# Kernel optimization log

Hardware: AMD Instinct MI355X
Metric: run time of the kernel (lower is better)

## Reference

```python
import jax, jax.numpy as jnp
import numpy as np

B, F, S, H = 8, 512, 8192, 8
D = F // H
GROUPS = F // 16  # GroupNorm group_cnt = channels // 16
EPS = 1e-8


def group_norm(x, gamma, beta):
    # x: [B, C, S]; normalize per (group-channels, spatial) like torch GroupNorm
    b, c, s = x.shape
    xg = x.reshape(b, GROUPS, c // GROUPS, s)
    mu = xg.mean(axis=(2, 3), keepdims=True)
    var = xg.var(axis=(2, 3), keepdims=True)
    xn = ((xg - mu) * jax.lax.rsqrt(var + EPS)).reshape(b, c, s)
    return xn * gamma[None, :, None] + beta[None, :, None]


def setup_inputs() -> dict:
    key = jax.random.key(0)
    ks = jax.random.split(key, 5)
    return {
        "hidden_states": jax.random.normal(ks[0], (B, F, S), jnp.float32),
        "qkv_w": jax.random.normal(ks[1], (3, H, D, F), jnp.float32) * 0.02,
        "qkv_b": jnp.zeros((3, 1, 1, H, D), jnp.float32),
        "out_proj": jax.random.normal(ks[2], (F, F), jnp.float32) * 0.02,
        "gn1_gamma": jnp.ones((F,), jnp.float32),
        "gn1_beta": jnp.zeros((F,), jnp.float32),
        "gn2_gamma": jnp.ones((F,), jnp.float32),
        "gn2_beta": jnp.zeros((F,), jnp.float32),
        # torch init is zeros; use small random so the gated branch is exercised
        "gate_g": jax.random.normal(ks[3], (F, 1), jnp.float32) * 0.1,
    }


def reference(hidden_states, qkv_w, qkv_b, out_proj,
              gn1_gamma, gn1_beta, gn2_gamma, gn2_beta, gate_g):
    x = group_norm(hidden_states, gn1_gamma, gn1_beta)
    # [3, B, S, H, D]
    qkv = jnp.einsum('bfl,ihdf->iblhd', x, qkv_w) + qkv_b
    q = jax.nn.elu(qkv[0]) + 1.0
    k = jax.nn.elu(qkv[1]) + 1.0
    v = qkv[2]
    # global non-causal linear attention: KV = sum_l k_l v_l^T  -> [B,H,D,D]
    kv = jnp.einsum('blhf,blhF->bhFf', k, v)
    k_sum = jnp.sum(k, axis=1, keepdims=True)               # [B,1,H,D]
    z = jnp.sum(q * k_sum, axis=-1, keepdims=True)          # [B,S,H,1]
    qz = q / z
    out = jnp.einsum('blhf,bhFf->blhF', qz, kv)             # [B,S,H,D]
    out = out.reshape(out.shape[0], out.shape[1], -1)       # [B,S,F]
    y = jnp.einsum('blf,Ff->bFl', out, out_proj)            # [B,F,S]
    y = group_norm(y, gn2_gamma, gn2_beta)
    # rezero-style gate: residual + per-channel gate * branch
    return hidden_states + gate_g[None] * y
```

## Files before the change

### kernel.cpp

```cpp
#include <hip/hip_runtime.h>
#include <hip/hip_bf16.h>

#define BB 8
#define FF 512
#define SS 8192
#define HH 8
#define DD 64
#define N1 1536

typedef __hip_bfloat16 bf16;
typedef __attribute__((ext_vector_type(8))) short bf16x8;
typedef __attribute__((ext_vector_type(4))) float f32x4;

__device__ __forceinline__ float us2f(unsigned short u) {
    union { unsigned int i; float f; } x; x.i = ((unsigned int)u) << 16; return x.f;
}
__device__ __forceinline__ unsigned short f2b(float f) {
    unsigned int u = __builtin_bit_cast(unsigned int, f);
    return (unsigned short)((u + 0x7FFFu + ((u >> 16) & 1u)) >> 16);
}
__device__ __forceinline__ void gll16(const void* g, void* l) {
    __builtin_amdgcn_global_load_lds((const __attribute__((address_space(1))) void*)g,
                                     (__attribute__((address_space(3))) void*)l, 16, 0, 0);
}
__device__ __forceinline__ bf16x8 fragld(const unsigned short* base, int row, int quad) {
    int off = row * 32 + (((quad + (row >> 1)) & 3) << 3);
    return *(const bf16x8*)(base + off);
}

__global__ void gn1_stats(const float* __restrict__ hid,
                          const float* __restrict__ gamma,
                          const float* __restrict__ beta,
                          float* __restrict__ sc, float* __restrict__ sh) {
    int bg = blockIdx.x;
    int b = bg >> 5, g = bg & 31;
    const float4* base = (const float4*)(hid + ((size_t)b * FF + g * 16) * SS);
    float s = 0.f, s2 = 0.f;
    for (int t = threadIdx.x; t < 32768; t += 256) {
        float4 x = base[t];
        s  += x.x + x.y + x.z + x.w;
        s2 += x.x * x.x + x.y * x.y + x.z * x.z + x.w * x.w;
    }
    #pragma unroll
    for (int off = 32; off > 0; off >>= 1) {
        s  += __shfl_down(s, off, 64);
        s2 += __shfl_down(s2, off, 64);
    }
    __shared__ float rs_[4], rs2_[4];
    int wid = threadIdx.x >> 6, lane = threadIdx.x & 63;
    if (lane == 0) { rs_[wid] = s; rs2_[wid] = s2; }
    __syncthreads();
    if (threadIdx.x < 16) {
        float ts  = rs_[0] + rs_[1] + rs_[2] + rs_[3];
        float ts2 = rs2_[0] + rs2_[1] + rs2_[2] + rs2_[3];
        float mu  = ts * (1.f / 131072.f);
        float var = ts2 * (1.f / 131072.f) - mu * mu;
        float r   = rsqrtf(var + 1e-8f);
        int c = g * 16 + threadIdx.x;
        float scv = gamma[c] * r;
        sc[b * FF + c] = scv;
        sh[b * FF + c] = beta[c] - mu * scv;
    }
}

__global__ void castb(const float* __restrict__ s, unsigned short* __restrict__ d, int n4) {
    int i = blockIdx.x * 256 + threadIdx.x;
    if (i >= n4) return;
    float4 v = ((const float4*)s)[i];
    ushort4 u = make_ushort4(f2b(v.x), f2b(v.y), f2b(v.z), f2b(v.w));
    ((ushort4*)d)[i] = u;
}

__global__ void xn_prep(const float* __restrict__ hid, const float* __restrict__ sc,
                        const float* __restrict__ sh, unsigned short* __restrict__ xnA) {
    int b = blockIdx.z, f0 = blockIdx.y * 64, l0 = blockIdx.x * 64;
    __shared__ float t[64][65];
    int tid = threadIdx.x;
    #pragma unroll
    for (int it = 0; it < 16; it++) {
        int idx = it * 256 + tid;
        int f = idx >> 6, l = idx & 63;
        int fg = f0 + f;
        t[f][l] = hid[((size_t)b * FF + fg) * SS + l0 + l] * sc[b * FF + fg] + sh[b * FF + fg];
    }
    __syncthreads();
    #pragma unroll
    for (int it = 0; it < 4; it++) {
        int idx = it * 256 + tid;
        int l = idx >> 4, fq = (idx & 15) * 4;
        ushort4 u = make_ushort4(f2b(t[fq + 0][l]), f2b(t[fq + 1][l]),
                                 f2b(t[fq + 2][l]), f2b(t[fq + 3][l]));
        *(ushort4*)(xnA + ((size_t)b * SS + l0 + l) * FF + f0 + fq) = u;
    }
}

__global__ __launch_bounds__(256) void gemm1_mfma(
    const unsigned short* __restrict__ A, const unsigned short* __restrict__ Bw,
    const float* __restrict__ bias,
    unsigned short* __restrict__ q, unsigned short* __restrict__ kT,
    unsigned short* __restrict__ vT) {
    __shared__ unsigned short As[128 * 32] __attribute__((aligned(16)));
    __shared__ unsigned short Bs[128 * 32] __attribute__((aligned(16)));
    const int b = blockIdx.z;
    const int m0 = blockIdx.x * 128, n0 = blockIdx.y * 128;
    const int tid = threadIdx.x;
    const int w = tid >> 6, ln = tid & 63;
    const int wr = w >> 1, wc = w & 1;
    const int lrow = ln & 15, quad = ln >> 4;

    const int ch0 = tid, ch1 = tid + 256;
    const int r0 = ch0 >> 2, c0 = ((ch0 & 3) - (r0 >> 1)) & 3;
    const int r1 = ch1 >> 2, c1 = ((ch1 & 3) - (r1 >> 1)) & 3;
    const unsigned short* pA0 = A + ((size_t)b * SS + m0 + r0) * FF + c0 * 8;
    const unsigned short* pA1 = A + ((size_t)b * SS + m0 + r1) * FF + c1 * 8;
    const unsigned short* pB0 = Bw + (size_t)(n0 + r0) * FF + c0 * 8;
    const unsigned short* pB1 = Bw + (size_t)(n0 + r1) * FF + c1 * 8;
    unsigned short* lA0 = As + ch0 * 8; unsigned short* lA1 = As + ch1 * 8;
    unsigned short* lB0 = Bs + ch0 * 8; unsigned short* lB1 = Bs + ch1 * 8;

    f32x4 acc[4][4];
    #pragma unroll
    for (int j = 0; j < 4; j++)
        #pragma unroll
        for (int i = 0; i < 4; i++) acc[j][i] = (f32x4){0.f, 0.f, 0.f, 0.f};

    for (int kk = 0; kk < 16; kk++) {
        gll16(pA0, lA0); gll16(pA1, lA1); gll16(pB0, lB0); gll16(pB1, lB1);
        pA0 += 32; pA1 += 32; pB0 += 32; pB1 += 32;
        __syncthreads();
        bf16x8 af[4], bm[4];
        #pragma unroll
        for (int j = 0; j < 4; j++) af[j] = fragld(Bs, wc * 64 + j * 16 + lrow, quad);
        #pragma unroll
        for (int i = 0; i < 4; i++) bm[i] = fragld(As, wr * 64 + i * 16 + lrow, quad);
        #pragma unroll
        for (int j = 0; j < 4; j++)
            #pragma unroll
            for (int i = 0; i < 4; i++)
                acc[j][i] = __builtin_amdgcn_mfma_f32_16x16x32_bf16(af[j], bm[i], acc[j][i], 0, 0, 0);
        __syncthreads();
    }
    const int n0v = n0 + wc * 64;
    const int sel = n0v >> 9;
    if (sel == 0) {
        const int rem0 = n0v & 511;
        const size_t mrow = (size_t)b * SS + m0 + wr * 64 + lrow;
        #pragma unroll
        for (int j = 0; j < 4; j++) {
            const float* bp = bias + n0v + j * 16 + (quad << 2);
            float b0 = bp[0], b1 = bp[1], b2 = bp[2], b3 = bp[3];
            #pragma unroll
            for (int i = 0; i < 4; i++) {
                float val0 = acc[j][i][0] + b0, val1 = acc[j][i][1] + b1;
                float val2 = acc[j][i][2] + b2, val3 = acc[j][i][3] + b3;
                val0 = val0 > 0.f ? val0 + 1.f : __expf(val0);
                val1 = val1 > 0.f ? val1 + 1.f : __expf(val1);
                val2 = val2 > 0.f ? val2 + 1.f : __expf(val2);
                val3 = val3 > 0.f ? val3 + 1.f : __expf(val3);
                ushort4 u = make_ushort4(f2b(val0), f2b(val1), f2b(val2), f2b(val3));
                *(ushort4*)(q + (mrow + i * 16) * FF + rem0 + j * 16 + (quad << 2)) = u;
            }
        }
    } else {
        unsigned short* outp = (sel == 1) ? kT : vT;
        const int nrel0 = (n0v & 511);
        const int lbase = m0 + wr * 64 + lrow;
        #pragma unroll
        for (int j = 0; j < 4; j++) {
            const float* bp = bias + n0v + j * 16 + (quad << 2);
            float bb4[4] = {bp[0], bp[1], bp[2], bp[3]};
            #pragma unroll
            for (int i = 0; i < 4; i++) {
                int l = lbase + i * 16;
                #pragma unroll
                for (int r = 0; r < 4; r++) {
                    float val = acc[j][i][r] + bb4[r];
                    if (sel == 1) val = val > 0.f ? val + 1.f : __expf(val);
                    int n = nrel0 + j * 16 + (quad << 2) + r;
                    int h = n >> 6, d = n & 63;
                    outp[(((size_t)b * HH + h) * DD + d) * SS + l] = f2b(val);
                }
            }
        }
    }
}

__global__ __launch_bounds__(256) void kv_mfma(
    const unsigned short* __restrict__ kT, const unsigned short* __restrict__ vT,
    float* __restrict__ kv, float* __restrict__ ksum) {
    const int bh = blockIdx.x;
    const int l0 = blockIdx.y * 512;
    const int tid = threadIdx.x;

    {
        int f = tid >> 2, part = tid & 3;
        const unsigned short* kp = kT + ((size_t)bh * DD + f) * SS + l0 + part * 128;
        float s = 0.f;
        #pragma unroll
        for (int c = 0; c < 16; c++) {
            bf16x8 u = *(const bf16x8*)(kp + c * 8);
            #pragma unroll
            for (int j = 0; j < 8; j++) s += us2f((unsigned short)u[j]);
        }
        s += __shfl_down(s, 1, 64);
        s += __shfl_down(s, 2, 64);
        if (part == 0) atomicAdd(&ksum[bh * DD + f], s);
    }

    const int w = tid >> 6, ln = tid & 63;
    const int lrow = ln & 15, quad = ln >> 4;
    f32x4 acc[4];
    #pragma unroll
    for (int ft = 0; ft < 4; ft++) acc[ft] = (f32x4){0.f, 0.f, 0.f, 0.f};
    const unsigned short* vbase = vT + ((size_t)bh * DD + w * 16 + lrow) * SS + l0;
    const unsigned short* kbase = kT + ((size_t)bh * DD + lrow) * SS + l0;
    for (int ks = 0; ks < 16; ks++) {
        bf16x8 vf = *(const bf16x8*)(vbase + ks * 32 + quad * 8);
        #pragma unroll
        for (int ft = 0; ft < 4; ft++) {
            bf16x8 kf = *(const bf16x8*)(kbase + (size_t)(ft * 16) * SS + ks * 32 + quad * 8);
            acc[ft] = __builtin_amdgcn_mfma_f32_16x16x32_bf16(vf, kf, acc[ft], 0, 0, 0);
        }
    }
    float* kvp = kv + (size_t)bh * 4096;
    #pragma unroll
    for (int ft = 0; ft < 4; ft++) {
        #pragma unroll
        for (int r = 0; r < 4; r++) {
            int e = w * 16 + (quad << 2) + r;
            int f = ft * 16 + lrow;
            atomicAdd(&kvp[e * 64 + f], acc[ft][r]);
        }
    }
}

__global__ void kvcast(const float* __restrict__ kv, unsigned short* __restrict__ kv16) {
    int i = blockIdx.x * 256 + threadIdx.x;
    float4 v = ((const float4*)kv)[i];
    ((ushort4*)kv16)[i] = make_ushort4(f2b(v.x), f2b(v.y), f2b(v.z), f2b(v.w));
}

__global__ __launch_bounds__(256) void attn_mfma(
    const unsigned short* __restrict__ q, const unsigned short* __restrict__ kv16,
    const float* __restrict__ ksum, unsigned short* __restrict__ attn) {
    const int bh = blockIdx.y, b = bh >> 3, h = bh & 7;
    const int l0 = blockIdx.x * 128;
    __shared__ float ksS[64];
    __shared__ float zS[128];
    const int tid = threadIdx.x;
    if (tid < 64) ksS[tid] = ksum[bh * DD + tid];
    __syncthreads();
    if (tid < 128) {
        const unsigned short* qp = q + ((size_t)b * SS + l0 + tid) * FF + h * DD;
        float z = 0.f;
        #pragma unroll
        for (int c = 0; c < 8; c++) {
            bf16x8 u = *(const bf16x8*)(qp + c * 8);
            #pragma unroll
            for (int j = 0; j < 8; j++) z += us2f((unsigned short)u[j]) * ksS[c * 8 + j];
        }
        zS[tid] = 1.f / z;
    }
    __syncthreads();

    const int w = tid >> 6, ln = tid & 63;
    const int lrow = ln & 15, quad = ln >> 4;
    const unsigned short* kvp = kv16 + (size_t)bh * 4096;
    bf16x8 kvf[4][2];
    #pragma unroll
    for (int et = 0; et < 4; et++)
        #pragma unroll
        for (int ks = 0; ks < 2; ks++)
            kvf[et][ks] = *(const bf16x8*)(kvp + (et * 16 + lrow) * 64 + ks * 32 + quad * 8);

    f32x4 acc[2][4];
    #pragma unroll
    for (int lt = 0; lt < 2; lt++)
        #pragma unroll
        for (int et = 0; et < 4; et++) acc[lt][et] = (f32x4){0.f, 0.f, 0.f, 0.f};

    const unsigned short* qbase = q + ((size_t)b * SS + l0 + w * 32) * FF + h * DD;
    #pragma unroll
    for (int lt = 0; lt < 2; lt++) {
        #pragma unroll
        for (int ks = 0; ks < 2; ks++) {
            bf16x8 qf = *(const bf16x8*)(qbase + (size_t)(lt * 16 + lrow) * FF + ks * 32 + quad * 8);
            #pragma unroll
            for (int et = 0; et < 4; et++)
                acc[lt][et] = __builtin_amdgcn_mfma_f32_16x16x32_bf16(kvf[et][ks], qf, acc[lt][et], 0, 0, 0);
        }
    }
    #pragma unroll
    for (int lt = 0; lt < 2; lt++) {
        int lloc = w * 32 + lt * 16 + lrow;
        float zi = zS[lloc];
        unsigned short* op = attn + ((size_t)b * SS + l0 + lloc) * FF + h * DD;
        #pragma unroll
        for (int et = 0; et < 4; et++) {
            ushort4 u = make_ushort4(f2b(acc[lt][et][0] * zi), f2b(acc[lt][et][1] * zi),
                                     f2b(acc[lt][et][2] * zi), f2b(acc[lt][et][3] * zi));
            *(ushort4*)(op + et * 16 + (quad << 2)) = u;
        }
    }
}

__global__ __launch_bounds__(256) void gemm2_mfma(
    const unsigned short* __restrict__ A, const unsigned short* __restrict__ Bw,
    unsigned short* __restrict__ y) {
    __shared__ unsigned short As[128 * 32] __attribute__((aligned(16)));
    __shared__ unsigned short Bs[128 * 32] __attribute__((aligned(16)));
    const int b = blockIdx.z;
    const int m0 = blockIdx.x * 128, n0 = blockIdx.y * 128;
    const int tid = threadIdx.x;
    const int w = tid >> 6, ln = tid & 63;
    const int wr = w >> 1, wc = w & 1;
    const int lrow = ln & 15, quad = ln >> 4;

    const int ch0 = tid, ch1 = tid + 256;
    const int r0 = ch0 >> 2, c0 = ((ch0 & 3) - (r0 >> 1)) & 3;
    const int r1 = ch1 >> 2, c1 = ((ch1 & 3) - (r1 >> 1)) & 3;
    const unsigned short* pA0 = A + ((size_t)b * SS + m0 + r0) * FF + c0 * 8;
    const unsigned short* pA1 = A + ((size_t)b * SS + m0 + r1) * FF + c1 * 8;
    const unsigned short* pB0 = Bw + (size_t)(n0 + r0) * FF + c0 * 8;
    const unsigned short* pB1 = Bw + (size_t)(n0 + r1) * FF + c1 * 8;
    unsigned short* lA0 = As + ch0 * 8; unsigned short* lA1 = As + ch1 * 8;
    unsigned short* lB0 = Bs + ch0 * 8; unsigned short* lB1 = Bs + ch1 * 8;

    f32x4 acc[4][4];
    #pragma unroll
    for (int i = 0; i < 4; i++)
        #pragma unroll
        for (int j = 0; j < 4; j++) acc[i][j] = (f32x4){0.f, 0.f, 0.f, 0.f};

    for (int kk = 0; kk < 16; kk++) {
        gll16(pA0, lA0); gll16(pA1, lA1); gll16(pB0, lB0); gll16(pB1, lB1);
        pA0 += 32; pA1 += 32; pB0 += 32; pB1 += 32;
        __syncthreads();
        bf16x8 am[4], bn[4];
        #pragma unroll
        for (int i = 0; i < 4; i++) am[i] = fragld(As, wr * 64 + i * 16 + lrow, quad);
        #pragma unroll
        for (int j = 0; j < 4; j++) bn[j] = fragld(Bs, wc * 64 + j * 16 + lrow, quad);
        #pragma unroll
        for (int i = 0; i < 4; i++)
            #pragma unroll
            for (int j = 0; j < 4; j++)
                acc[i][j] = __builtin_amdgcn_mfma_f32_16x16x32_bf16(am[i], bn[j], acc[i][j], 0, 0, 0);
        __syncthreads();
    }
    const int nb = n0 + wc * 64 + lrow;
    const int lb0 = m0 + wr * 64 + (quad << 2);
    #pragma unroll
    for (int i = 0; i < 4; i++) {
        #pragma unroll
        for (int j = 0; j < 4; j++) {
            ushort4 u = make_ushort4(f2b(acc[i][j][0]), f2b(acc[i][j][1]),
                                     f2b(acc[i][j][2]), f2b(acc[i][j][3]));
            *(ushort4*)(y + ((size_t)b * FF + nb + j * 16) * SS + lb0 + i * 16) = u;
        }
    }
}

__global__ void gn2_stats(const bf16* __restrict__ y, const float* __restrict__ gamma,
                          const float* __restrict__ beta, const float* __restrict__ gate,
                          float* __restrict__ gsc, float* __restrict__ gsh) {
    int bg = blockIdx.x;
    int b = bg >> 5, g = bg & 31;
    const ushort4* base = (const ushort4*)(y + ((size_t)b * FF + g * 16) * SS);
    float s = 0.f, s2 = 0.f;
    for (int t = threadIdx.x; t < 32768; t += 256) {
        ushort4 u = base[t];
        float a0 = us2f(u.x), a1 = us2f(u.y), a2 = us2f(u.z), a3 = us2f(u.w);
        s  += a0 + a1 + a2 + a3;
        s2 += a0 * a0 + a1 * a1 + a2 * a2 + a3 * a3;
    }
    #pragma unroll
    for (int off = 32; off > 0; off >>= 1) {
        s  += __shfl_down(s, off, 64);
        s2 += __shfl_down(s2, off, 64);
    }
    __shared__ float rs_[4], rs2_[4];
    int wid = threadIdx.x >> 6, lane = threadIdx.x & 63;
    if (lane == 0) { rs_[wid] = s; rs2_[wid] = s2; }
    __syncthreads();
    if (threadIdx.x < 16) {
        float ts  = rs_[0] + rs_[1] + rs_[2] + rs_[3];
        float ts2 = rs2_[0] + rs2_[1] + rs2_[2] + rs2_[3];
        float mu  = ts * (1.f / 131072.f);
        float var = ts2 * (1.f / 131072.f) - mu * mu;
        float r   = rsqrtf(var + 1e-8f);
        int c = g * 16 + threadIdx.x;
        float scv = gamma[c] * r;
        gsc[b * FF + c] = gate[c] * scv;
        gsh[b * FF + c] = gate[c] * (beta[c] - mu * scv);
    }
}

__global__ void final_kernel(const float* __restrict__ hid, const bf16* __restrict__ y,
                             const float* __restrict__ gsc, const float* __restrict__ gsh,
                             float* __restrict__ out) {
    int bf = blockIdx.x;
    float a = gsc[bf], c0 = gsh[bf];
    const float4*  hp = (const float4*)(hid + (size_t)bf * SS);
    const ushort4* yp = (const ushort4*)(y + (size_t)bf * SS);
    float4* op = (float4*)(out + (size_t)bf * SS);
    for (int t = threadIdx.x; t < 2048; t += 256) {
        float4 hv = hp[t];
        ushort4 yv = yp[t];
        float4 r;
        r.x = hv.x + a * us2f(yv.x) + c0;
        r.y = hv.y + a * us2f(yv.y) + c0;
        r.z = hv.z + a * us2f(yv.z) + c0;
        r.w = hv.w + a * us2f(yv.w) + c0;
        op[t] = r;
    }
}

extern "C" void kernel_launch(void* const* d_in, const int* in_sizes, int n_in,
                              void* d_out, int out_size, void* d_ws, size_t ws_size,
                              hipStream_t stream) {
    const float* hid      = (const float*)d_in[0];
    const float* qkv_w    = (const float*)d_in[1];
    const float* qkv_b    = (const float*)d_in[2];
    const float* out_proj = (const float*)d_in[3];
    const float* g1       = (const float*)d_in[4];
    const float* b1       = (const float*)d_in[5];
    const float* g2       = (const float*)d_in[6];
    const float* b2       = (const float*)d_in[7];
    const float* gate     = (const float*)d_in[8];
    float* out = (float*)d_out;

    char* p = (char*)d_ws;
    float* sc1 = (float*)p; p += (size_t)4096 * 4;
    float* sh1 = (float*)p; p += (size_t)4096 * 4;
    float* gsc = (float*)p; p += (size_t)4096 * 4;
    float* gsh = (float*)p; p += (size_t)4096 * 4;
    float* kvb = (float*)p; p += (size_t)262144 * 4;
    float* ksm = (float*)p; p += (size_t)4096 * 4;
    unsigned short* kv16 = (unsigned short*)p; p += (size_t)262144 * 2;
    unsigned short* Wb = (unsigned short*)p; p += (size_t)786432 * 2;
    unsigned short* Pb = (unsigned short*)p; p += (size_t)262144 * 2;
    unsigned short* qb = (unsigned short*)p; p += (size_t)33554432 * 2;
    unsigned short* kTb = (unsigned short*)p; p += (size_t)33554432 * 2;
    unsigned short* vTb = (unsigned short*)p;
    unsigned short* attn = kTb;
    unsigned short* yb   = vTb;
    unsigned short* xnA  = (unsigned short*)d_out;

    hipMemsetAsync(kvb, 0, (size_t)(262144 + 4096) * 4, stream);

    gn1_stats<<<256, 256, 0, stream>>>(hid, g1, b1, sc1, sh1);
    castb<<<768, 256, 0, stream>>>(qkv_w, Wb, 196608);
    castb<<<256, 256, 0, stream>>>(out_proj, Pb, 65536);
    xn_prep<<<dim3(128, 8, 8), 256, 0, stream>>>(hid, sc1, sh1, xnA);
    gemm1_mfma<<<dim3(64, 12, 8), 256, 0, stream>>>(xnA, Wb, qkv_b, qb, kTb, vTb);
    kv_mfma<<<dim3(64, 16), 256, 0, stream>>>(kTb, vTb, kvb, ksm);
    kvcast<<<256, 256, 0, stream>>>(kvb, kv16);
    attn_mfma<<<dim3(64, 64), 256, 0, stream>>>(qb, kv16, ksm, attn);
    gemm2_mfma<<<dim3(64, 4, 8), 256, 0, stream>>>(attn, Pb, yb);
    gn2_stats<<<256, 256, 0, stream>>>((const bf16*)yb, g2, b2, gate, gsc, gsh);
    final_kernel<<<4096, 256, 0, stream>>>(hid, (const bf16*)yb, gsc, gsh, out);
}
```

Before: 729.8 us.

## Split GroupNorm stats across more blocks; stage GEMM epilogues through LDS for coalesced stores

Each GroupNorm statistics pass is split over 8x more blocks. Partial sums are combined with atomics and finished by a small separate kernel, so the 128 MB fp32 and bf16 reductions use the whole GPU instead of 256 blocks. The gemm1 and gemm2 epilogues now write tiles into a swizzled LDS buffer and then issue 16-byte coalesced global stores. This replaces the scattered 2-byte transposed stores for kT/vT and the strided 8-byte stores. The cost is extra launches, atomics, a larger shared memory footprint (32 KB) that may lower occupancy, and an extra sync in the epilogues.

```diff
diff --git a/kernel.cpp b/kernel.cpp
--- a/kernel.cpp
+++ b/kernel.cpp
@@ -28,16 +28,14 @@
     return *(const bf16x8*)(base + off);
 }
 
-__global__ void gn1_stats(const float* __restrict__ hid,
-                          const float* __restrict__ gamma,
-                          const float* __restrict__ beta,
-                          float* __restrict__ sc, float* __restrict__ sh) {
+__global__ void gn1_part(const float* __restrict__ hid, float* __restrict__ part) {
     int bg = blockIdx.x;
-    int b = bg >> 5, g = bg & 31;
-    const float4* base = (const float4*)(hid + ((size_t)b * FF + g * 16) * SS);
+    const float4* base = (const float4*)(hid + ((size_t)(bg >> 5) * FF + (bg & 31) * 16) * SS);
     float s = 0.f, s2 = 0.f;
-    for (int t = threadIdx.x; t < 32768; t += 256) {
-        float4 x = base[t];
+    int t0 = blockIdx.y * 4096 + threadIdx.x;
+    #pragma unroll
+    for (int it = 0; it < 16; it++) {
+        float4 x = base[t0 + it * 256];
         s  += x.x + x.y + x.z + x.w;
         s2 += x.x * x.x + x.y * x.y + x.z * x.z + x.w * x.w;
     }
@@ -46,21 +44,59 @@
         s  += __shfl_down(s, off, 64);
         s2 += __shfl_down(s2, off, 64);
     }
-    __shared__ float rs_[4], rs2_[4];
+    __shared__ float rs_[8];
     int wid = threadIdx.x >> 6, lane = threadIdx.x & 63;
-    if (lane == 0) { rs_[wid] = s; rs2_[wid] = s2; }
-    __syncthreads();
-    if (threadIdx.x < 16) {
-        float ts  = rs_[0] + rs_[1] + rs_[2] + rs_[3];
-        float ts2 = rs2_[0] + rs2_[1] + rs2_[2] + rs2_[3];
-        float mu  = ts * (1.f / 131072.f);
-        float var = ts2 * (1.f / 131072.f) - mu * mu;
-        float r   = rsqrtf(var + 1e-8f);
-        int c = g * 16 + threadIdx.x;
-        float scv = gamma[c] * r;
-        sc[b * FF + c] = scv;
-        sh[b * FF + c] = beta[c] - mu * scv;
-    }
+    if (lane == 0) { rs_[wid] = s; rs_[wid + 4] = s2; }
+    __syncthreads();
+    if (threadIdx.x == 0)
+        atomicAdd(&part[bg * 2], rs_[0] + rs_[1] + rs_[2] + rs_[3]);
+    else if (threadIdx.x == 64)
+        atomicAdd(&part[bg * 2 + 1], rs_[4] + rs_[5] + rs_[6] + rs_[7]);
+}
+
+__global__ void gn2_part(const unsigned short* __restrict__ y, float* __restrict__ part) {
+    int bg = blockIdx.x;
+    const bf16x8* base = (const bf16x8*)(y + ((size_t)(bg >> 5) * FF + (bg & 31) * 16) * SS);
+    float s = 0.f, s2 = 0.f;
+    int t0 = blockIdx.y * 2048 + threadIdx.x;
+    #pragma unroll
+    for (int it = 0; it < 8; it++) {
+        bf16x8 u = base[t0 + it * 256];
+        #pragma unroll
+        for (int k = 0; k < 8; k++) {
+            float a = us2f((unsigned short)u[k]);
+            s += a; s2 += a * a;
+        }
+    }
+    #pragma unroll
+    for (int off = 32; off > 0; off >>= 1) {
+        s  += __shfl_down(s, off, 64);
+        s2 += __shfl_down(s2, off, 64);
+    }
+    __shared__ float rs_[8];
+    int wid = threadIdx.x >> 6, lane = threadIdx.x & 63;
+    if (lane == 0) { rs_[wid] = s; rs_[wid + 4] = s2; }
+    __syncthreads();
+    if (threadIdx.x == 0)
+        atomicAdd(&part[bg * 2], rs_[0] + rs_[1] + rs_[2] + rs_[3]);
+    else if (threadIdx.x == 64)
+        atomicAdd(&part[bg * 2 + 1], rs_[4] + rs_[5] + rs_[6] + rs_[7]);
+}
+
+__global__ void gn_final(const float* __restrict__ part, const float* __restrict__ gamma,
+                         const float* __restrict__ beta, const float* __restrict__ gate,
+                         float* __restrict__ sc, float* __restrict__ sh) {
+    int c = blockIdx.x * 256 + threadIdx.x;
+    int ch = c & 511;
+    int bg = (c >> 9) * 32 + (ch >> 4);
+    float ts = part[bg * 2], ts2 = part[bg * 2 + 1];
+    float mu  = ts * (1.f / 131072.f);
+    float var = ts2 * (1.f / 131072.f) - mu * mu;
+    float r   = rsqrtf(var + 1e-8f);
+    float scv = gamma[ch] * r;
+    float shv = beta[ch] - mu * scv;
+    if (gate) { float gv = gate[ch]; scv *= gv; shv *= gv; }
+    sc[c] = scv; sh[c] = shv;
 }
 
 __global__ void castb(const float* __restrict__ s, unsigned short* __restrict__ d, int n4) {
@@ -99,8 +135,9 @@
     const float* __restrict__ bias,
     unsigned short* __restrict__ q, unsigned short* __restrict__ kT,
     unsigned short* __restrict__ vT) {
-    __shared__ unsigned short As[128 * 32] __attribute__((aligned(16)));
-    __shared__ unsigned short Bs[128 * 32] __attribute__((aligned(16)));
+    __shared__ unsigned short smem[16384] __attribute__((aligned(16)));
+    unsigned short* As = smem;
+    unsigned short* Bs = smem + 4096;
     const int b = blockIdx.z;
     const int m0 = blockIdx.x * 128, n0 = blockIdx.y * 128;
     const int tid = threadIdx.x;
@@ -141,46 +178,66 @@
         __syncthreads();
     }
     const int n0v = n0 + wc * 64;
-    const int sel = n0v >> 9;
+    const int sel = n0 >> 9;
     if (sel == 0) {
-        const int rem0 = n0v & 511;
-        const size_t mrow = (size_t)b * SS + m0 + wr * 64 + lrow;
+        const int nchb = (wc << 3) + (quad >> 1);
+        const int nin  = (quad & 1) << 2;
         #pragma unroll
         for (int j = 0; j < 4; j++) {
             const float* bp = bias + n0v + j * 16 + (quad << 2);
             float b0 = bp[0], b1 = bp[1], b2 = bp[2], b3 = bp[3];
             #pragma unroll
             for (int i = 0; i < 4; i++) {
-                float val0 = acc[j][i][0] + b0, val1 = acc[j][i][1] + b1;
-                float val2 = acc[j][i][2] + b2, val3 = acc[j][i][3] + b3;
-                val0 = val0 > 0.f ? val0 + 1.f : __expf(val0);
-                val1 = val1 > 0.f ? val1 + 1.f : __expf(val1);
-                val2 = val2 > 0.f ? val2 + 1.f : __expf(val2);
-                val3 = val3 > 0.f ? val3 + 1.f : __expf(val3);
-                ushort4 u = make_ushort4(f2b(val0), f2b(val1), f2b(val2), f2b(val3));
-                *(ushort4*)(q + (mrow + i * 16) * FF + rem0 + j * 16 + (quad << 2)) = u;
+                float v0 = acc[j][i][0] + b0, v1 = acc[j][i][1] + b1;
+                float v2 = acc[j][i][2] + b2, v3 = acc[j][i][3] + b3;
+                v0 = v0 > 0.f ? v0 + 1.f : __expf(v0);
+                v1 = v1 > 0.f ? v1 + 1.f : __expf(v1);
+                v2 = v2 > 0.f ? v2 + 1.f : __expf(v2);
+                v3 = v3 > 0.f ? v3 + 1.f : __expf(v3);
+                int m = (wr << 6) + (i << 4) + lrow;
+                int chk = (nchb + (j << 1)) ^ (m & 7);
+                *(ushort4*)(smem + m * 128 + (chk << 3) + nin) =
+                    make_ushort4(f2b(v0), f2b(v1), f2b(v2), f2b(v3));
             }
+        }
+        __syncthreads();
+        const size_t rowb = (size_t)b * SS + m0;
+        const int cc = tid & 15, rr = tid >> 4;
+        #pragma unroll
+        for (int p = 0; p < 8; p++) {
+            int m = (p << 4) + rr;
+            bf16x8 v = *(const bf16x8*)(smem + m * 128 + ((cc ^ (m & 7)) << 3));
+            *(bf16x8*)(q + (rowb + m) * FF + n0 + (cc << 3)) = v;
         }
     } else {
         unsigned short* outp = (sel == 1) ? kT : vT;
-        const int nrel0 = (n0v & 511);
-        const int lbase = m0 + wr * 64 + lrow;
+        const int nbase = n0 & 511;
         #pragma unroll
         for (int j = 0; j < 4; j++) {
             const float* bp = bias + n0v + j * 16 + (quad << 2);
-            float bb4[4] = {bp[0], bp[1], bp[2], bp[3]};
+            float bb[4] = {bp[0], bp[1], bp[2], bp[3]};
             #pragma unroll
             for (int i = 0; i < 4; i++) {
-                int l = lbase + i * 16;
+                int m = (wr << 6) + (i << 4) + lrow;
+                int mch = m >> 3, mi = m & 7;
                 #pragma unroll
                 for (int r = 0; r < 4; r++) {
-                    float val = acc[j][i][r] + bb4[r];
+                    float val = acc[j][i][r] + bb[r];
                     if (sel == 1) val = val > 0.f ? val + 1.f : __expf(val);
-                    int n = nrel0 + j * 16 + (quad << 2) + r;
-                    int h = n >> 6, d = n & 63;
-                    outp[(((size_t)b * HH + h) * DD + d) * SS + l] = f2b(val);
+                    int n = (wc << 6) + (j << 4) + (quad << 2) + r;
+                    smem[n * 128 + ((mch ^ ((n >> 2) & 7)) << 3) + mi] = f2b(val);
                 }
             }
+        }
+        __syncthreads();
+        const int cc = tid & 15, rr = tid >> 4;
+        #pragma unroll
+        for (int p = 0; p < 8; p++) {
+            int n = (p << 4) + rr;
+            bf16x8 v = *(const bf16x8*)(smem + n * 128 + ((cc ^ ((n >> 2) & 7)) << 3));
+            int nrel = nbase + n;
+            *(bf16x8*)(outp + (((size_t)b * HH + (nrel >> 6)) * DD + (nrel & 63)) * SS
+                       + m0 + (cc << 3)) = v;
         }
     }
 }
@@ -307,8 +364,9 @@
 __global__ __launch_bounds__(256) void gemm2_mfma(
     const unsigned short* __restrict__ A, const unsigned short* __restrict__ Bw,
     unsigned short* __restrict__ y) {
-    __shared__ unsigned short As[128 * 32] __attribute__((aligned(16)));
-    __shared__ unsigned short Bs[128 * 32] __attribute__((aligned(16)));
+    __shared__ unsigned short smem[16384] __attribute__((aligned(16)));
+    unsigned short* As = smem;
+    unsigned short* Bs = smem + 4096;
     const int b = blockIdx.z;
     const int m0 = blockIdx.x * 128, n0 = blockIdx.y * 128;
     const int tid = threadIdx.x;
@@ -348,51 +406,26 @@
                 acc[i][j] = __builtin_amdgcn_mfma_f32_16x16x32_bf16(am[i], bn[j], acc[i][j], 0, 0, 0);
         __syncthreads();
     }
-    const int nb = n0 + wc * 64 + lrow;
-    const int lb0 = m0 + wr * 64 + (quad << 2);
     #pragma unroll
     for (int i = 0; i < 4; i++) {
+        const int mch = (wr << 3) + (i << 1) + (quad >> 1);
+        const int min_ = (quad & 1) << 2;
         #pragma unroll
         for (int j = 0; j < 4; j++) {
-            ushort4 u = make_ushort4(f2b(acc[i][j][0]), f2b(acc[i][j][1]),
-                                     f2b(acc[i][j][2]), f2b(acc[i][j][3]));
-            *(ushort4*)(y + ((size_t)b * FF + nb + j * 16) * SS + lb0 + i * 16) = u;
-        }
-    }
-}
-
-__global__ void gn2_stats(const bf16* __restrict__ y, const float* __restrict__ gamma,
-                          const float* __restrict__ beta, const float* __restrict__ gate,
-                          float* __restrict__ gsc, float* __restrict__ gsh) {
-    int bg = blockIdx.x;
-    int b = bg >> 5, g = bg & 31;
-    const ushort4* base = (const ushort4*)(y + ((size_t)b * FF + g * 16) * SS);
-    float s = 0.f, s2 = 0.f;
-    for (int t = threadIdx.x; t < 32768; t += 256) {
-        ushort4 u = base[t];
-        float a0 = us2f(u.x), a1 = us2f(u.y), a2 = us2f(u.z), a3 = us2f(u.w);
-        s  += a0 + a1 + a2 + a3;
-        s2 += a0 * a0 + a1 * a1 + a2 * a2 + a3 * a3;
-    }
-    #pragma unroll
-    for (int off = 32; off > 0; off >>= 1) {
-        s  += __shfl_down(s, off, 64);
-        s2 += __shfl_down(s2, off, 64);
-    }
-    __shared__ float rs_[4], rs2_[4];
-    int wid = threadIdx.x >> 6, lane = threadIdx.x & 63;
-    if (lane == 0) { rs_[wid] = s; rs2_[wid] = s2; }
-    __syncthreads();
-    if (threadIdx.x < 16) {
-        float ts  = rs_[0] + rs_[1] + rs_[2] + rs_[3];
-        float ts2 = rs2_[0] + rs2_[1] + rs2_[2] + rs2_[3];
-        float mu  = ts * (1.f / 131072.f);
-        float var = ts2 * (1.f / 131072.f) - mu * mu;
-        float r   = rsqrtf(var + 1e-8f);
-        int c = g * 16 + threadIdx.x;
-        float scv = gamma[c] * r;
-        gsc[b * FF + c] = gate[c] * scv;
-        gsh[b * FF + c] = gate[c] * (beta[c] - mu * scv);
+            int n = (wc << 6) + (j << 4) + lrow;
+            int chk = mch ^ (n & 7);
+            *(ushort4*)(smem + n * 128 + (chk << 3) + min_) =
+                make_ushort4(f2b(acc[i][j][0]), f2b(acc[i][j][1]),
+                             f2b(acc[i][j][2]), f2b(acc[i][j][3]));
+        }
+    }
+    __syncthreads();
+    const int cc = tid & 15, rr = tid >> 4;
+    #pragma unroll
+    for (int p = 0; p < 8; p++) {
+        int n = (p << 4) + rr;
+        bf16x8 v = *(const bf16x8*)(smem + n * 128 + ((cc ^ (n & 7)) << 3));
+        *(bf16x8*)(y + ((size_t)b * FF + n0 + n) * SS + m0 + (cc << 3)) = v;
     }
 }
 
@@ -437,6 +470,7 @@
     float* gsh = (float*)p; p += (size_t)4096 * 4;
     float* kvb = (float*)p; p += (size_t)262144 * 4;
     float* ksm = (float*)p; p += (size_t)4096 * 4;
+    float* gnp = (float*)p; p += (size_t)1024 * 4;
     unsigned short* kv16 = (unsigned short*)p; p += (size_t)262144 * 2;
     unsigned short* Wb = (unsigned short*)p; p += (size_t)786432 * 2;
     unsigned short* Pb = (unsigned short*)p; p += (size_t)262144 * 2;
@@ -447,9 +481,10 @@
     unsigned short* yb   = vTb;
     unsigned short* xnA  = (unsigned short*)d_out;
 
-    hipMemsetAsync(kvb, 0, (size_t)(262144 + 4096) * 4, stream);
-
-    gn1_stats<<<256, 256, 0, stream>>>(hid, g1, b1, sc1, sh1);
+    hipMemsetAsync(kvb, 0, (size_t)(262144 + 4096 + 1024) * 4, stream);
+
+    gn1_part<<<dim3(256, 8), 256, 0, stream>>>(hid, gnp);
+    gn_final<<<16, 256, 0, stream>>>(gnp, g1, b1, nullptr, sc1, sh1);
     castb<<<768, 256, 0, stream>>>(qkv_w, Wb, 196608);
     castb<<<256, 256, 0, stream>>>(out_proj, Pb, 65536);
     xn_prep<<<dim3(128, 8, 8), 256, 0, stream>>>(hid, sc1, sh1, xnA);
@@ -458,6 +493,7 @@
     kvcast<<<256, 256, 0, stream>>>(kvb, kv16);
     attn_mfma<<<dim3(64, 64), 256, 0, stream>>>(qb, kv16, ksm, attn);
     gemm2_mfma<<<dim3(64, 4, 8), 256, 0, stream>>>(attn, Pb, yb);
-    gn2_stats<<<256, 256, 0, stream>>>((const bf16*)yb, g2, b2, gate, gsc, gsh);
+    gn2_part<<<dim3(256, 8), 256, 0, stream>>>((const unsigned short*)yb, gnp + 512);
+    gn_final<<<16, 256, 0, stream>>>(gnp + 512, g2, b2, gate, gsc, gsh);
     final_kernel<<<4096, 256, 0, stream>>>(hid, (const bf16*)yb, gsc, gsh, out);
 }
```

Result: faster. 651.6 us (-10.7%).
